# Kernel tuning notes

Measured on AMD Instinct MI355X. Metric: run time of the kernel, lower is better.

## Reference

```python
import jax, jax.numpy as jnp
import numpy as np

B, S, K, N = 4, 2048, 4096, 4096
BLK = 32  # Q4_0 block size along the K (input) dimension


def setup_inputs() -> dict:
    key = jax.random.key(0)
    k1, k2, k3, k4 = jax.random.split(key, 4)
    x = jax.random.normal(k1, (B, S, K), dtype=jnp.float32)
    # 4-bit codes stored unpacked as int32 in [0, 16)
    qweight = jax.random.randint(k2, (N, K), 0, 16, dtype=jnp.int32)
    # one positive fp scale per 32-wide block (typical Q4_0 magnitudes)
    scales = jax.random.uniform(k3, (N, K // BLK), dtype=jnp.float32) * 0.1
    bias = jax.random.normal(k4, (N,), dtype=jnp.float32)
    return {"x": x, "qweight": qweight, "scales": scales, "bias": bias}


def dequantize_q4_0(qweight, scales):
    # w[n, k] = scale[n, k//32] * (q[n, k] - 8)
    n, k = qweight.shape
    q = qweight.reshape(n, k // BLK, BLK).astype(scales.dtype)
    w = (q - 8.0) * scales[:, :, None]
    return w.reshape(n, k)


def reference(x, qweight, scales, bias):
    # dequantize once (cached path), then F.linear(x, w, bias)
    w = dequantize_q4_0(qweight, scales)          # [N, K]
    out = jnp.einsum("bsk,nk->bsn", x, w)          # [B, S, N]
    return out + bias
```

## Files before the change

kernel.cpp:

```cpp
#include <hip/hip_runtime.h>
#include <stdint.h>

#define M_DIM 8192
#define N_DIM 4096
#define K_DIM 4096
#define NKB   (K_DIM / 32)
#define BK    64
#define KT    (K_DIM / BK)
#define ITERS (KT / 2)
#define GRID_WGS ((M_DIM / 256) * (N_DIM / 256))

typedef __bf16 bf16x8 __attribute__((ext_vector_type(8)));
typedef float  f32x4  __attribute__((ext_vector_type(4)));

__device__ __forceinline__ uint32_t pack2_bf16(float lo, float hi) {
    union { float f; uint32_t u; } a, b;
    a.f = lo; b.f = hi;
    return __builtin_amdgcn_perm(b.u + 0x8000u, a.u + 0x8000u, 0x07060302u);
}


__global__ void cvt_x_kernel(const float* __restrict__ x,
                             uint32_t* __restrict__ xb, int n8) {
    int i = blockIdx.x * blockDim.x + threadIdx.x;
    if (i >= n8) return;
    const float4* p = (const float4*)x;
    float4 v0 = p[2 * i], v1 = p[2 * i + 1];
    uint4 o;
    o.x = pack2_bf16(v0.x, v0.y);
    o.y = pack2_bf16(v0.z, v0.w);
    o.z = pack2_bf16(v1.x, v1.y);
    o.w = pack2_bf16(v1.z, v1.w);
    ((uint4*)xb)[i] = o;
}

__global__ void dequant_kernel(const int* __restrict__ q,
                               const float* __restrict__ s,
                               uint32_t* __restrict__ wb, int n8) {
    int i = blockIdx.x * blockDim.x + threadIdx.x;
    if (i >= n8) return;
    int base = i << 3;
    int n = base >> 12;
    int k = base & (K_DIM - 1);
    float sc = s[n * NKB + (k >> 5)];
    float m8 = -8.0f * sc;
    const int4* qp = (const int4*)q;
    int4 q0 = qp[2 * i], q1 = qp[2 * i + 1];
    uint4 o;
    o.x = pack2_bf16(fmaf((float)q0.x, sc, m8), fmaf((float)q0.y, sc, m8));
    o.y = pack2_bf16(fmaf((float)q0.z, sc, m8), fmaf((float)q0.w, sc, m8));
    o.z = pack2_bf16(fmaf((float)q1.x, sc, m8), fmaf((float)q1.y, sc, m8));
    o.w = pack2_bf16(fmaf((float)q1.z, sc, m8), fmaf((float)q1.w, sc, m8));
    ((uint4*)wb)[i] = o;
}

__global__ __launch_bounds__(512, 2)
void gemm_bf16_256_kernel(const __bf16* __restrict__ A,
                          const __bf16* __restrict__ Bw,
                          const float* __restrict__ bias,
                          float* __restrict__ C) {
    __shared__ __align__(16) __bf16 lds[8][128 * 64];

    const int t    = threadIdx.x;
    const int wave = t >> 6;
    const int lane = t & 63;
    const int wm = wave >> 2;
    const int wn = wave & 3;

    const int flat = blockIdx.x;
    const int wgid = (flat & 7) * (GRID_WGS / 8) + (flat >> 3);
    const int bm = wgid >> 4;
    const int bn = wgid & 15;

    const __bf16* Ab = A  + (size_t)bm * 256 * K_DIM;
    const __bf16* Bb = Bw + (size_t)bn * 256 * K_DIM;

    const int rr0 = t >> 3;
    const int cg  = (t & 7) ^ (rr0 & 7);
    const size_t aoff = (size_t)rr0 * K_DIM + cg * 8;
    const size_t boff = (size_t)((rr0 >> 5) * 64 + (rr0 & 31)) * K_DIM + cg * 8;

#define STAGE(ktg, unit)                                                      \
    do {                                                                      \
        const __bf16* _s;                                                     \
        __bf16* _d;                                                           \
        if ((unit) == 0 || (unit) == 3) {                                     \
            const int _mh = ((unit) == 3) ? 1 : 0;                            \
            _s = Ab + (size_t)_mh * 64 * K_DIM + (size_t)(ktg) * 64 + aoff;   \
            _d = &lds[((ktg) & 1) * 4 + _mh][0] + t * 8;                      \
        } else {                                                              \
            const int _nh = ((unit) == 2) ? 1 : 0;                            \
            _s = Bb + (size_t)_nh * 32 * K_DIM + (size_t)(ktg) * 64 + boff;   \
            _d = &lds[((ktg) & 1) * 4 + 2 + _nh][0] + t * 8;                  \
        }                                                                     \
        __builtin_amdgcn_global_load_lds(                                     \
            (const __attribute__((address_space(1))) uint32_t*)_s,            \
            (__attribute__((address_space(3))) uint32_t*)_d, 16, 0, 0);       \
        __builtin_amdgcn_global_load_lds(                                     \
            (const __attribute__((address_space(1))) uint32_t*)               \
                (_s + (size_t)128 * K_DIM),                                   \
            (__attribute__((address_space(3))) uint32_t*)(_d + 4096),         \
            16, 0, 0);                                                        \
    } while (0)

    const int r = lane & 15, quad = lane >> 4;
    const int s0 = quad ^ (r & 7);
    const int aRow = (wm * 64 + r) * 64;
    const int bRow = (wn * 32 + r) * 64;

    bf16x8 a[4][2], b0[2][2], b1[2][2];
    f32x4 acc[8][4] = {};

#define LOAD_A(buf, mh)                                                       \
    do { const __bf16* _p = &lds[(buf) * 4 + (mh)][aRow];                     \
        _Pragma("unroll") for (int i2 = 0; i2 < 4; ++i2) {                    \
            a[i2][0] = *(const bf16x8*)(_p + i2 * 1024 + s0 * 8);             \
            a[i2][1] = *(const bf16x8*)(_p + i2 * 1024 + (s0 ^ 4) * 8);       \
        } } while (0)

#define LOAD_B(dst, buf, nh)                                                  \
    do { const __bf16* _p = &lds[(buf) * 4 + 2 + (nh)][bRow];                 \
        _Pragma("unroll") for (int j2 = 0; j2 < 2; ++j2) {                    \
            dst[j2][0] = *(const bf16x8*)(_p + j2 * 1024 + s0 * 8);           \
            dst[j2][1] = *(const bf16x8*)(_p + j2 * 1024 + (s0 ^ 4) * 8);     \
        } } while (0)

#define MFMA16(IB, BSEL, JB)                                                  \
    do { __builtin_amdgcn_s_setprio(1);                                       \
        _Pragma("unroll") for (int i2 = 0; i2 < 4; ++i2)                      \
        _Pragma("unroll") for (int j2 = 0; j2 < 2; ++j2)                      \
        _Pragma("unroll") for (int h = 0; h < 2; ++h)                         \
            acc[(IB) + i2][(JB) + j2] =                                       \
                __builtin_amdgcn_mfma_f32_16x16x32_bf16(                      \
                    a[i2][h], BSEL[j2][h], acc[(IB) + i2][(JB) + j2],         \
                    0, 0, 0);                                                 \
        __builtin_amdgcn_s_setprio(0); } while (0)

#define BAR() do { asm volatile("" ::: "memory");                             \
                   __builtin_amdgcn_s_barrier();                              \
                   asm volatile("" ::: "memory"); } while (0)
#define VMCNT(n) asm volatile("s_waitcnt vmcnt(" #n ")" ::: "memory")

    STAGE(0, 0); STAGE(0, 1); STAGE(0, 2); STAGE(0, 3);
    STAGE(1, 0); STAGE(1, 1); STAGE(1, 2);
    VMCNT(6);
    BAR();

#define KBODY(it, LAST)                                                       \
    do {                                                                      \
        const int _k0 = 2 * (it);                                             \
                             \
        LOAD_A(0, 0); LOAD_B(b0, 0, 0);                                       \
        STAGE(_k0 + 1, 3);                                                    \
        BAR(); MFMA16(0, b0, 0); BAR();                                       \
                         \
        LOAD_B(b1, 0, 1);                                                     \
        if (!(LAST)) STAGE(_k0 + 2, 0);                                       \
        BAR(); MFMA16(0, b1, 2); BAR();                                       \
                       \
        LOAD_A(0, 1);                                                         \
        if (!(LAST)) STAGE(_k0 + 2, 1);                                       \
        BAR(); MFMA16(4, b1, 2); BAR();                                       \
         \
        if (!(LAST)) STAGE(_k0 + 2, 2);                                       \
        BAR(); MFMA16(4, b0, 0);                                              \
        if (LAST) { VMCNT(0); } else { VMCNT(6); }                            \
        BAR();                                                                \
                          \
        LOAD_A(1, 0); LOAD_B(b0, 1, 0);                                       \
        if (!(LAST)) STAGE(_k0 + 2, 3);                                       \
        BAR(); MFMA16(0, b0, 0); BAR();                                       \
                         \
        LOAD_B(b1, 1, 1);                                                     \
        if (!(LAST)) STAGE(_k0 + 3, 0);                                       \
        BAR(); MFMA16(0, b1, 2); BAR();                                       \
                               \
        LOAD_A(1, 1);                                                         \
        if (!(LAST)) STAGE(_k0 + 3, 1);                                       \
        BAR(); MFMA16(4, b1, 2); BAR();                                       \
         \
        if (!(LAST)) STAGE(_k0 + 3, 2);                                       \
        BAR(); MFMA16(4, b0, 0);                                              \
        if (!(LAST)) { VMCNT(6); }                                            \
        BAR();                                                                \
    } while (0)

#pragma unroll 1
    for (int it = 0; it < ITERS - 1; ++it) KBODY(it, 0);
    KBODY(ITERS - 1, 1);

#undef KBODY
#undef STAGE
#undef LOAD_A
#undef LOAD_B
#undef MFMA16
#undef BAR
#undef VMCNT

    const int m0 = bm * 256 + wm * 128;
    const int n0 = bn * 256 + wn * 64;
#pragma unroll
    for (int j = 0; j < 4; ++j) {
        const int col = n0 + j * 16 + r;
        const float bv = bias[col];
#pragma unroll
        for (int i = 0; i < 8; ++i) {
            const int rbase = m0 + i * 16 + quad * 4;
#pragma unroll
            for (int e = 0; e < 4; ++e)
                C[(size_t)(rbase + e) * N_DIM + col] = acc[i][j][e] + bv;
        }
    }
}

__global__ __launch_bounds__(256)
void fused_gemm_kernel(const float* __restrict__ X,
                       const int* __restrict__ Q,
                       const float* __restrict__ S,
                       const float* __restrict__ bias,
                       float* __restrict__ C) {
    __shared__ __align__(16) __bf16 lA[128 * 32];
    __shared__ __align__(16) __bf16 lB[128 * 32];

    const int t    = threadIdx.x;
    const int wave = t >> 6;
    const int lane = t & 63;
    const int bm = blockIdx.y, bn = blockIdx.x;
    const int wm = wave >> 1, wn = wave & 1;

    const int srow = t >> 1;
    const int sc0  = (t & 1) << 4;
    const float* gX = X + (size_t)(bm * 128 + srow) * K_DIM + sc0;
    const int*   gQ = Q + (size_t)(bn * 128 + srow) * K_DIM + sc0;
    const float* gS = S + (size_t)(bn * 128 + srow) * NKB;
    __bf16* sA = lA + srow * 32 + sc0;
    __bf16* sB = lB + srow * 32 + sc0;

    const int r = lane & 15, quad = lane >> 4;
    const __bf16* fA = lA + (wm * 64 + r) * 32 + quad * 8;
    const __bf16* fB = lB + (wn * 64 + r) * 32 + quad * 8;

    f32x4 acc[4][4] = {};

    float4 x0 = ((const float4*)gX)[0];
    float4 x1 = ((const float4*)gX)[1];
    float4 x2 = ((const float4*)gX)[2];
    float4 x3 = ((const float4*)gX)[3];
    int4 q0 = ((const int4*)gQ)[0];
    int4 q1 = ((const int4*)gQ)[1];
    int4 q2 = ((const int4*)gQ)[2];
    int4 q3 = ((const int4*)gQ)[3];
    float sc = gS[0];

    for (int kt = 0; kt < NKB; ++kt) {
        uint4 pa0, pa1, pb0, pb1;
        pa0.x = pack2_bf16(x0.x, x0.y); pa0.y = pack2_bf16(x0.z, x0.w);
        pa0.z = pack2_bf16(x1.x, x1.y); pa0.w = pack2_bf16(x1.z, x1.w);
        pa1.x = pack2_bf16(x2.x, x2.y); pa1.y = pack2_bf16(x2.z, x2.w);
        pa1.z = pack2_bf16(x3.x, x3.y); pa1.w = pack2_bf16(x3.z, x3.w);
        float m8 = -8.0f * sc;
        pb0.x = pack2_bf16(fmaf((float)q0.x, sc, m8), fmaf((float)q0.y, sc, m8));
        pb0.y = pack2_bf16(fmaf((float)q0.z, sc, m8), fmaf((float)q0.w, sc, m8));
        pb0.z = pack2_bf16(fmaf((float)q1.x, sc, m8), fmaf((float)q1.y, sc, m8));
        pb0.w = pack2_bf16(fmaf((float)q1.z, sc, m8), fmaf((float)q1.w, sc, m8));
        pb1.x = pack2_bf16(fmaf((float)q2.x, sc, m8), fmaf((float)q2.y, sc, m8));
        pb1.y = pack2_bf16(fmaf((float)q2.z, sc, m8), fmaf((float)q2.w, sc, m8));
        pb1.z = pack2_bf16(fmaf((float)q3.x, sc, m8), fmaf((float)q3.y, sc, m8));
        pb1.w = pack2_bf16(fmaf((float)q3.z, sc, m8), fmaf((float)q3.w, sc, m8));

        __syncthreads();
        *(uint4*)sA = pa0; *(uint4*)(sA + 8) = pa1;
        *(uint4*)sB = pb0; *(uint4*)(sB + 8) = pb1;
        __syncthreads();

        if (kt + 1 < NKB) {
            gX += 32; gQ += 32;
            x0 = ((const float4*)gX)[0];
            x1 = ((const float4*)gX)[1];
            x2 = ((const float4*)gX)[2];
            x3 = ((const float4*)gX)[3];
            q0 = ((const int4*)gQ)[0];
            q1 = ((const int4*)gQ)[1];
            q2 = ((const int4*)gQ)[2];
            q3 = ((const int4*)gQ)[3];
            sc = gS[kt + 1];
        }

        bf16x8 af[4], bfr[4];
#pragma unroll
        for (int i = 0; i < 4; ++i)
            af[i] = *(const bf16x8*)(fA + i * 16 * 32);
#pragma unroll
        for (int j = 0; j < 4; ++j)
            bfr[j] = *(const bf16x8*)(fB + j * 16 * 32);
#pragma unroll
        for (int i = 0; i < 4; ++i)
#pragma unroll
            for (int j = 0; j < 4; ++j)
                acc[i][j] = __builtin_amdgcn_mfma_f32_16x16x32_bf16(
                    af[i], bfr[j], acc[i][j], 0, 0, 0);
    }

    const int m0 = bm * 128 + wm * 64;
    const int n0 = bn * 128 + wn * 64;
#pragma unroll
    for (int j = 0; j < 4; ++j) {
        int col = n0 + j * 16 + r;
        float bv = bias[col];
#pragma unroll
        for (int i = 0; i < 4; ++i) {
            int rbase = m0 + i * 16 + quad * 4;
#pragma unroll
            for (int e = 0; e < 4; ++e)
                C[(size_t)(rbase + e) * N_DIM + col] = acc[i][j][e] + bv;
        }
    }
}

extern "C" void kernel_launch(void* const* d_in, const int* in_sizes, int n_in,
                              void* d_out, int out_size, void* d_ws, size_t ws_size,
                              hipStream_t stream) {
    const float* x    = (const float*)d_in[0];
    const int*   qw   = (const int*)d_in[1];
    const float* sc   = (const float*)d_in[2];
    const float* bias = (const float*)d_in[3];
    float* out = (float*)d_out;

    const size_t need = ((size_t)M_DIM * K_DIM + (size_t)N_DIM * K_DIM) * 2;
    if (ws_size >= need && d_ws != nullptr) {
        uint32_t* xb = (uint32_t*)d_ws;
        uint32_t* wb = xb + (size_t)M_DIM * K_DIM / 2;
        int n8x = M_DIM * K_DIM / 8;
        cvt_x_kernel<<<n8x / 256, 256, 0, stream>>>(x, xb, n8x);
        int n8w = N_DIM * K_DIM / 8;
        dequant_kernel<<<n8w / 256, 256, 0, stream>>>(qw, sc, wb, n8w);
        gemm_bf16_256_kernel<<<dim3(GRID_WGS), dim3(512), 0, stream>>>(
            (const __bf16*)xb, (const __bf16*)wb, bias, out);
    } else {
        dim3 grid(N_DIM / 128, M_DIM / 128);
        fused_gemm_kernel<<<grid, 256, 0, stream>>>(x, qw, sc, bias, out);
    }
}
```

Baseline: 481.9 us.

## Switch GEMM to 32x32x16 MFMA tiles and merge prep kernels into one grid-stride launch

The bf16 GEMM inner loop moves from 16x16x32 MFMA instructions to 32x32x16 ones, with new LDS read patterns, an accumulator layout of 4x2 f32x16 per wave, and a matching epilogue store mapping. Larger MFMA tiles cut the number of instructions and the LDS reads needed per FLOP. Separately, the x-conversion and weight-dequant kernels are merged into one grid-stride prep kernel to save a launch. The risks are LDS bank conflicts under the new XOR swizzle indexing and the more strided pattern of the epilogue stores.

```diff
diff --git a/kernel.cpp b/kernel.cpp
--- a/kernel.cpp
+++ b/kernel.cpp
@@ -10,8 +10,13 @@
 #define ITERS (KT / 2)
 #define GRID_WGS ((M_DIM / 256) * (N_DIM / 256))
 
+#define X8_TOTAL (M_DIM * K_DIM / 8)
+#define W8_TOTAL (N_DIM * K_DIM / 8)
+#define PREP_BLOCKS 2048
+
 typedef __bf16 bf16x8 __attribute__((ext_vector_type(8)));
 typedef float  f32x4  __attribute__((ext_vector_type(4)));
+typedef float  f32x16 __attribute__((ext_vector_type(16)));
 
 __device__ __forceinline__ uint32_t pack2_bf16(float lo, float hi) {
     union { float f; uint32_t u; } a, b;
@@ -19,39 +24,41 @@
     return __builtin_amdgcn_perm(b.u + 0x8000u, a.u + 0x8000u, 0x07060302u);
 }
 
-
-__global__ void cvt_x_kernel(const float* __restrict__ x,
-                             uint32_t* __restrict__ xb, int n8) {
-    int i = blockIdx.x * blockDim.x + threadIdx.x;
-    if (i >= n8) return;
-    const float4* p = (const float4*)x;
-    float4 v0 = p[2 * i], v1 = p[2 * i + 1];
-    uint4 o;
-    o.x = pack2_bf16(v0.x, v0.y);
-    o.y = pack2_bf16(v0.z, v0.w);
-    o.z = pack2_bf16(v1.x, v1.y);
-    o.w = pack2_bf16(v1.z, v1.w);
-    ((uint4*)xb)[i] = o;
-}
-
-__global__ void dequant_kernel(const int* __restrict__ q,
-                               const float* __restrict__ s,
-                               uint32_t* __restrict__ wb, int n8) {
-    int i = blockIdx.x * blockDim.x + threadIdx.x;
-    if (i >= n8) return;
-    int base = i << 3;
-    int n = base >> 12;
-    int k = base & (K_DIM - 1);
-    float sc = s[n * NKB + (k >> 5)];
-    float m8 = -8.0f * sc;
-    const int4* qp = (const int4*)q;
-    int4 q0 = qp[2 * i], q1 = qp[2 * i + 1];
-    uint4 o;
-    o.x = pack2_bf16(fmaf((float)q0.x, sc, m8), fmaf((float)q0.y, sc, m8));
-    o.y = pack2_bf16(fmaf((float)q0.z, sc, m8), fmaf((float)q0.w, sc, m8));
-    o.z = pack2_bf16(fmaf((float)q1.x, sc, m8), fmaf((float)q1.y, sc, m8));
-    o.w = pack2_bf16(fmaf((float)q1.z, sc, m8), fmaf((float)q1.w, sc, m8));
-    ((uint4*)wb)[i] = o;
+__global__ __launch_bounds__(256)
+void prep_kernel(const float* __restrict__ x,
+                 const int* __restrict__ q,
+                 const float* __restrict__ s,
+                 uint32_t* __restrict__ xb,
+                 uint32_t* __restrict__ wb) {
+    const int stride = gridDim.x * 256;
+    for (int idx = blockIdx.x * 256 + threadIdx.x;
+         idx < X8_TOTAL + W8_TOTAL; idx += stride) {
+        if (idx < X8_TOTAL) {
+            const float4* p = (const float4*)x;
+            float4 v0 = p[2 * idx], v1 = p[2 * idx + 1];
+            uint4 o;
+            o.x = pack2_bf16(v0.x, v0.y);
+            o.y = pack2_bf16(v0.z, v0.w);
+            o.z = pack2_bf16(v1.x, v1.y);
+            o.w = pack2_bf16(v1.z, v1.w);
+            ((uint4*)xb)[idx] = o;
+        } else {
+            const int i = idx - X8_TOTAL;
+            const int base = i << 3;
+            const int n = base >> 12;
+            const int k = base & (K_DIM - 1);
+            float sc = s[n * NKB + (k >> 5)];
+            float m8 = -8.0f * sc;
+            const int4* qp = (const int4*)q;
+            int4 q0 = qp[2 * i], q1 = qp[2 * i + 1];
+            uint4 o;
+            o.x = pack2_bf16(fmaf((float)q0.x, sc, m8), fmaf((float)q0.y, sc, m8));
+            o.y = pack2_bf16(fmaf((float)q0.z, sc, m8), fmaf((float)q0.w, sc, m8));
+            o.z = pack2_bf16(fmaf((float)q1.x, sc, m8), fmaf((float)q1.y, sc, m8));
+            o.w = pack2_bf16(fmaf((float)q1.z, sc, m8), fmaf((float)q1.w, sc, m8));
+            ((uint4*)wb)[i] = o;
+        }
+    }
 }
 
 __global__ __launch_bounds__(512, 2)
@@ -103,37 +110,37 @@
             16, 0, 0);                                                        \
     } while (0)
 
-    const int r = lane & 15, quad = lane >> 4;
-    const int s0 = quad ^ (r & 7);
-    const int aRow = (wm * 64 + r) * 64;
-    const int bRow = (wn * 32 + r) * 64;
-
-    bf16x8 a[4][2], b0[2][2], b1[2][2];
-    f32x4 acc[8][4] = {};
-
-#define LOAD_A(buf, mh)                                                       \
-    do { const __bf16* _p = &lds[(buf) * 4 + (mh)][aRow];                     \
-        _Pragma("unroll") for (int i2 = 0; i2 < 4; ++i2) {                    \
-            a[i2][0] = *(const bf16x8*)(_p + i2 * 1024 + s0 * 8);             \
-            a[i2][1] = *(const bf16x8*)(_p + i2 * 1024 + (s0 ^ 4) * 8);       \
+    const int l31 = lane & 31;
+    const int hi  = lane >> 5;
+    const int l7  = lane & 7;
+    const int aR0 = (wm * 64 + l31) * 64;
+    const int bR  = (wn * 32 + l31) * 64;
+
+    bf16x8 a[2][4], b0[4], b1[4];
+    f32x16 acc[4][2] = {};
+
+#define LOAD_A32(buf, mh)                                                     \
+    do { const __bf16* _p = &lds[(buf) * 4 + (mh)][0];                        \
+        _Pragma("unroll") for (int hf = 0; hf < 2; ++hf) {                    \
+            const __bf16* _q = _p + aR0 + hf * 32 * 64;                       \
+            _Pragma("unroll") for (int ks = 0; ks < 4; ++ks)                  \
+                a[hf][ks] =                                                   \
+                    *(const bf16x8*)(_q + ((ks * 2 + hi) ^ l7) * 8);          \
         } } while (0)
 
-#define LOAD_B(dst, buf, nh)                                                  \
-    do { const __bf16* _p = &lds[(buf) * 4 + 2 + (nh)][bRow];                 \
-        _Pragma("unroll") for (int j2 = 0; j2 < 2; ++j2) {                    \
-            dst[j2][0] = *(const bf16x8*)(_p + j2 * 1024 + s0 * 8);           \
-            dst[j2][1] = *(const bf16x8*)(_p + j2 * 1024 + (s0 ^ 4) * 8);     \
-        } } while (0)
-
-#define MFMA16(IB, BSEL, JB)                                                  \
+#define LOAD_B32(dst, buf, nh)                                                \
+    do { const __bf16* _p = &lds[(buf) * 4 + 2 + (nh)][bR];                   \
+        _Pragma("unroll") for (int ks = 0; ks < 4; ++ks)                      \
+            dst[ks] = *(const bf16x8*)(_p + ((ks * 2 + hi) ^ l7) * 8);        \
+    } while (0)
+
+#define MFMA8(MH, BSEL, NT)                                                   \
     do { __builtin_amdgcn_s_setprio(1);                                       \
-        _Pragma("unroll") for (int i2 = 0; i2 < 4; ++i2)                      \
-        _Pragma("unroll") for (int j2 = 0; j2 < 2; ++j2)                      \
-        _Pragma("unroll") for (int h = 0; h < 2; ++h)                         \
-            acc[(IB) + i2][(JB) + j2] =                                       \
-                __builtin_amdgcn_mfma_f32_16x16x32_bf16(                      \
-                    a[i2][h], BSEL[j2][h], acc[(IB) + i2][(JB) + j2],         \
-                    0, 0, 0);                                                 \
+        _Pragma("unroll") for (int hf = 0; hf < 2; ++hf)                      \
+        _Pragma("unroll") for (int ks = 0; ks < 4; ++ks)                      \
+            acc[(MH) * 2 + hf][NT] =                                          \
+                __builtin_amdgcn_mfma_f32_32x32x16_bf16(                      \
+                    a[hf][ks], BSEL[ks], acc[(MH) * 2 + hf][NT], 0, 0, 0);    \
         __builtin_amdgcn_s_setprio(0); } while (0)
 
 #define BAR() do { asm volatile("" ::: "memory");                             \
@@ -149,38 +156,38 @@
 #define KBODY(it, LAST)                                                       \
     do {                                                                      \
         const int _k0 = 2 * (it);                                             \
-                             \
-        LOAD_A(0, 0); LOAD_B(b0, 0, 0);                                       \
+                         \
+        LOAD_A32(0, 0); LOAD_B32(b0, 0, 0);                                   \
         STAGE(_k0 + 1, 3);                                                    \
-        BAR(); MFMA16(0, b0, 0); BAR();                                       \
-                         \
-        LOAD_B(b1, 0, 1);                                                     \
+        BAR(); MFMA8(0, b0, 0); BAR();                                        \
+                     \
+        LOAD_B32(b1, 0, 1);                                                   \
         if (!(LAST)) STAGE(_k0 + 2, 0);                                       \
-        BAR(); MFMA16(0, b1, 2); BAR();                                       \
-                       \
-        LOAD_A(0, 1);                                                         \
+        BAR(); MFMA8(0, b1, 1); BAR();                                        \
+                   \
+        LOAD_A32(0, 1);                                                       \
         if (!(LAST)) STAGE(_k0 + 2, 1);                                       \
-        BAR(); MFMA16(4, b1, 2); BAR();                                       \
-         \
+        BAR(); MFMA8(1, b1, 1); BAR();                                        \
+           \
         if (!(LAST)) STAGE(_k0 + 2, 2);                                       \
-        BAR(); MFMA16(4, b0, 0);                                              \
+        BAR(); MFMA8(1, b0, 0);                                               \
         if (LAST) { VMCNT(0); } else { VMCNT(6); }                            \
         BAR();                                                                \
-                          \
-        LOAD_A(1, 0); LOAD_B(b0, 1, 0);                                       \
+                      \
+        LOAD_A32(1, 0); LOAD_B32(b0, 1, 0);                                   \
         if (!(LAST)) STAGE(_k0 + 2, 3);                                       \
-        BAR(); MFMA16(0, b0, 0); BAR();                                       \
-                         \
-        LOAD_B(b1, 1, 1);                                                     \
+        BAR(); MFMA8(0, b0, 0); BAR();                                        \
+                     \
+        LOAD_B32(b1, 1, 1);                                                   \
         if (!(LAST)) STAGE(_k0 + 3, 0);                                       \
-        BAR(); MFMA16(0, b1, 2); BAR();                                       \
-                               \
-        LOAD_A(1, 1);                                                         \
+        BAR(); MFMA8(0, b1, 1); BAR();                                        \
+                           \
+        LOAD_A32(1, 1);                                                       \
         if (!(LAST)) STAGE(_k0 + 3, 1);                                       \
-        BAR(); MFMA16(4, b1, 2); BAR();                                       \
-         \
+        BAR(); MFMA8(1, b1, 1); BAR();                                        \
+           \
         if (!(LAST)) STAGE(_k0 + 3, 2);                                       \
-        BAR(); MFMA16(4, b0, 0);                                              \
+        BAR(); MFMA8(1, b0, 0);                                               \
         if (!(LAST)) { VMCNT(6); }                                            \
         BAR();                                                                \
     } while (0)
@@ -191,24 +198,26 @@
 
 #undef KBODY
 #undef STAGE
-#undef LOAD_A
-#undef LOAD_B
-#undef MFMA16
+#undef LOAD_A32
+#undef LOAD_B32
+#undef MFMA8
 #undef BAR
 #undef VMCNT
 
     const int m0 = bm * 256 + wm * 128;
     const int n0 = bn * 256 + wn * 64;
 #pragma unroll
-    for (int j = 0; j < 4; ++j) {
-        const int col = n0 + j * 16 + r;
+    for (int nt = 0; nt < 2; ++nt) {
+        const int col = n0 + nt * 32 + l31;
         const float bv = bias[col];
 #pragma unroll
-        for (int i = 0; i < 8; ++i) {
-            const int rbase = m0 + i * 16 + quad * 4;
-#pragma unroll
-            for (int e = 0; e < 4; ++e)
-                C[(size_t)(rbase + e) * N_DIM + col] = acc[i][j][e] + bv;
+        for (int mt = 0; mt < 4; ++mt) {
+            const int rb = m0 + mt * 32 + 4 * hi;
+#pragma unroll
+            for (int reg = 0; reg < 16; ++reg) {
+                const int row = rb + (reg & 3) + 8 * (reg >> 2);
+                C[(size_t)row * N_DIM + col] = acc[mt][nt][reg] + bv;
+            }
         }
     }
 }
@@ -330,10 +339,7 @@
     if (ws_size >= need && d_ws != nullptr) {
         uint32_t* xb = (uint32_t*)d_ws;
         uint32_t* wb = xb + (size_t)M_DIM * K_DIM / 2;
-        int n8x = M_DIM * K_DIM / 8;
-        cvt_x_kernel<<<n8x / 256, 256, 0, stream>>>(x, xb, n8x);
-        int n8w = N_DIM * K_DIM / 8;
-        dequant_kernel<<<n8w / 256, 256, 0, stream>>>(qw, sc, wb, n8w);
+        prep_kernel<<<PREP_BLOCKS, 256, 0, stream>>>(x, qw, sc, xb, wb);
         gemm_bf16_256_kernel<<<dim3(GRID_WGS), dim3(512), 0, stream>>>(
             (const __bf16*)xb, (const __bf16*)wb, bias, out);
     } else {
```

New measurement: 514.4 us. 1.07x slower.
